# Optimization experiments

Hardware: AMD Instinct MI355X
Metric: run time of the kernel (lower is better)

## Reference

```python
import jax, jax.numpy as jnp
import numpy as np

N, E, D, G, C = 50000, 800000, 128, 64, 2
SCALE = 1.0 / np.sqrt(D).astype(np.float32)


def setup_inputs() -> dict:
    key = jax.random.key(0)
    ks = jax.random.split(key, 32)
    inp = {
        "x": jax.random.normal(ks[0], (N, D), dtype=jnp.float32),
        "edge_index": jax.random.randint(ks[1], (2, E), 0, N),
        "batch": jnp.sort(jax.random.randint(ks[2], (N,), 0, G)),
    }
    i = 3
    for l in range(2):
        for nm in ("Wq", "Wk", "Wv", "Ws"):
            inp[f"{nm}{l}"] = jax.random.normal(ks[i], (D, D), dtype=jnp.float32) * 0.05
            i += 1
        for nm in ("bq", "bk", "bv", "bs"):
            inp[f"{nm}{l}"] = jnp.zeros((D,), dtype=jnp.float32)
    inp["Wc1"] = jax.random.normal(ks[i], (D // 2, D), dtype=jnp.float32) * 0.05
    inp["bc1"] = jnp.zeros((D // 2,), dtype=jnp.float32)
    inp["Wc2"] = jax.random.normal(ks[i + 1], (C, D // 2), dtype=jnp.float32) * 0.05
    inp["bc2"] = jnp.zeros((C,), dtype=jnp.float32)
    return inp


def _transformer_conv(x, src, dst, Wq, bq, Wk, bk, Wv, bv, Ws, bs):
    # PyG TransformerConv, heads=1, concat=True, root_weight=True, beta=False.
    q = x @ Wq.T + bq            # [N, D] node-level projections, then gather per edge
    k = x @ Wk.T + bk
    v = x @ Wv.T + bv
    alpha = jnp.sum(q[dst] * k[src], axis=-1) * SCALE          # [E]
    # segment softmax over incoming edges of each target node
    m = jax.ops.segment_max(alpha, dst, num_segments=N)         # [N]
    ea = jnp.exp(alpha - m[dst])
    denom = jax.ops.segment_sum(ea, dst, num_segments=N)        # [N]
    w = ea / denom[dst]                                         # [E]
    out = jax.ops.segment_sum(v[src] * w[:, None], dst, num_segments=N)  # [N, D]
    return out + x @ Ws.T + bs   # skip connection (lin_skip)


def reference(x, edge_index, batch,
              Wq0, bq0, Wk0, bk0, Wv0, bv0, Ws0, bs0,
              Wq1, bq1, Wk1, bk1, Wv1, bv1, Ws1, bs1,
              Wc1, bc1, Wc2, bc2):
    src, dst = edge_index[0], edge_index[1]
    h = _transformer_conv(x, src, dst, Wq0, bq0, Wk0, bk0, Wv0, bv0, Ws0, bs0)
    h = jax.nn.relu(h)  # dropout is a no-op in eval mode
    h = _transformer_conv(h, src, dst, Wq1, bq1, Wk1, bk1, Wv1, bv1, Ws1, bs1)
    h = jax.nn.relu(h)
    # global mean pool over graphs
    sums = jax.ops.segment_sum(h, batch, num_segments=G)        # [G, D]
    cnts = jax.ops.segment_sum(jnp.ones((h.shape[0],), h.dtype), batch, num_segments=G)
    pooled = sums / jnp.maximum(cnts, 1.0)[:, None]
    # classifier MLP: [D -> D//2 -> C]
    z = jax.nn.relu(pooled @ Wc1.T + bc1)
    return z @ Wc2.T + bc2
```

## Files before the change

kernel.cpp:

```cpp
#include <hip/hip_runtime.h>
#include <math.h>

typedef __bf16 bf16x8 __attribute__((ext_vector_type(8)));
typedef float  f32x4  __attribute__((ext_vector_type(4)));
typedef float  f32x2  __attribute__((ext_vector_type(2)));
typedef unsigned short ushort_t;
typedef unsigned short ushort8 __attribute__((ext_vector_type(8)));

constexpr int Nn = 50000;
constexpr int Ee = 800000;
constexpr int Dd = 128;
constexpr int Gg = 64;
constexpr float SCALE = 0.08838834764831845f;
constexpr float QS    = 16.0f;
constexpr float ISC   = SCALE / (QS * QS);

__device__ inline ushort_t f2bf(float f) {
    unsigned u = __float_as_uint(f);
    unsigned r = (u + 0x7FFF + ((u >> 16) & 1)) >> 16;
    return (ushort_t)r;
}
__device__ inline float bf2f(ushort_t b) { return __uint_as_float(((unsigned)b) << 16); }

__device__ inline char q_i8(float f) {
    int v = (int)rintf(f * QS);
    v = max(-127, min(127, v));
    return (char)v;
}


constexpr int EB  = (Ee + 255) / 256;
constexpr int NBD = (Nn + 255) / 256;
constexpr int CWB = 64;
constexpr int N4  = Nn * Dd / 4;
constexpr int CXB = N4 / 256;

__global__ __launch_bounds__(256) void prep_kernel(
    const int* __restrict__ dst, int* __restrict__ counts, int* __restrict__ rank,
    const int* __restrict__ batch, int* __restrict__ startg, int* __restrict__ endg,
    const float* w0, const float* w1, const float* w2, const float* w3,
    const float* w4, const float* w5, const float* w6, const float* w7,
    ushort_t* __restrict__ Wfh, ushort_t* __restrict__ Wfl,
    const float* __restrict__ x, ushort_t* __restrict__ Xh, ushort_t* __restrict__ Xl) {
    int b = blockIdx.x;
    if (b < EB) {
        int e = b * 256 + threadIdx.x;
        if (e < Ee) rank[e] = atomicAdd(&counts[dst[e]], 1);
    } else if (b < EB + NBD) {
        int n = (b - EB) * 256 + threadIdx.x;
        if (n >= Nn) return;
        int g = batch[n];
        if (n == Nn - 1 || batch[n + 1] != g) endg[g] = n + 1;
        if (n == 0 || batch[n - 1] != g) startg[g] = n;
    } else if (b < EB + NBD + CWB) {
        const float* ws[8] = {w0, w1, w2, w3, w4, w5, w6, w7};
        int b2 = b - (EB + NBD);
        int m = b2 >> 3;
        int tt = (b2 & 7) * 256 + threadIdx.x;
        int lane = tt & 63;
        int ln = lane & 15, quad = lane >> 4;
        int n = (tt >> 9) * 32 + ((tt >> 8) & 1) * 16 + ln;
        int k0 = ((tt >> 6) & 3) * 32 + quad * 8;
        const float* srcp = ws[m] + n * 128 + k0;
        float4 a = *(const float4*)(srcp);
        float4 bb = *(const float4*)(srcp + 4);
        float e[8] = {a.x, a.y, a.z, a.w, bb.x, bb.y, bb.z, bb.w};
        ushort8 h, l;
#pragma unroll
        for (int j = 0; j < 8; ++j) {
            h[j] = f2bf(e[j]);
            l[j] = f2bf(e[j] - bf2f(h[j]));
        }
        size_t o = (size_t)m * 16384 + (size_t)tt * 8;
        *(ushort8*)(Wfh + o) = h;
        *(ushort8*)(Wfl + o) = l;
    } else {
        int i = (b - (EB + NBD + CWB)) * 256 + threadIdx.x;
        if (i >= N4) return;
        float4 xv = ((const float4*)x)[i];
        ushort4 h, l;
        h.x = f2bf(xv.x); l.x = f2bf(xv.x - bf2f(h.x));
        h.y = f2bf(xv.y); l.y = f2bf(xv.y - bf2f(h.y));
        h.z = f2bf(xv.z); l.z = f2bf(xv.z - bf2f(h.z));
        h.w = f2bf(xv.w); l.w = f2bf(xv.w - bf2f(h.w));
        ((ushort4*)Xh)[i] = h;
        ((ushort4*)Xl)[i] = l;
    }
}


__global__ __launch_bounds__(256) void scan1_kernel(const int* __restrict__ counts,
                                                    int* __restrict__ offsets,
                                                    int* __restrict__ blockSums) {
    __shared__ int sh[256];
    int i = blockIdx.x * 256 + threadIdx.x;
    int v = (i < Nn) ? counts[i] : 0;
    sh[threadIdx.x] = v;
    __syncthreads();
    for (int off = 1; off < 256; off <<= 1) {
        int t = (threadIdx.x >= off) ? sh[threadIdx.x - off] : 0;
        __syncthreads();
        sh[threadIdx.x] += t;
        __syncthreads();
    }
    if (i < Nn) offsets[i] = sh[threadIdx.x] - v;
    if (threadIdx.x == 255) blockSums[blockIdx.x] = sh[255];
}

__global__ __launch_bounds__(256) void scan2_kernel(int* __restrict__ blockSums, int nb) {
    __shared__ int sh[256];
    int t = threadIdx.x;
    int v = (t < nb) ? blockSums[t] : 0;
    sh[t] = v;
    __syncthreads();
    for (int off = 1; off < 256; off <<= 1) {
        int u = (t >= off) ? sh[t - off] : 0;
        __syncthreads();
        sh[t] += u;
        __syncthreads();
    }
    if (t < nb) blockSums[t] = sh[t] - v;
}

__global__ __launch_bounds__(256) void scan3_kernel(int* __restrict__ offsets,
                                                    const int* __restrict__ blockSums) {
    int i = blockIdx.x * 256 + threadIdx.x;
    if (i < Nn) offsets[i] += blockSums[blockIdx.x];
    if (i == 0) offsets[Nn] = Ee;
}


constexpr int XS = 136;

__device__ __attribute__((always_inline)) void gemm_body(int bx, int which,
    const ushort_t* __restrict__ Xh, const ushort_t* __restrict__ Xl,
    const ushort_t* __restrict__ Wfh, const ushort_t* __restrict__ Wfl,
    int lw,
    const float* __restrict__ b0, const float* __restrict__ b1,
    const float* __restrict__ b2, const float* __restrict__ b3,
    char* __restrict__ Oq, char* __restrict__ Okv,
    ushort_t* __restrict__ Os) {
    __shared__ ushort_t XhS[64 * XS];
    __shared__ ushort_t XlS[64 * XS];
    const ushort_t* wfh = Wfh + (size_t)(lw + which) * 16384;
    const ushort_t* wfl = Wfl + (size_t)(lw + which) * 16384;
    const float* bias = (which == 0) ? b0 : (which == 1) ? b1 : (which == 2) ? b2 : b3;
    char* O8 = (which == 0) ? Oq : (which == 1) ? Okv : Okv + 128;
    int   o8str = (which == 0) ? 128 : 256;

    int w = threadIdx.x >> 6;
    int lane = threadIdx.x & 63;
    int quad = lane >> 4, ln = lane & 15;
    int n0 = w * 32;

    bf16x8 bh[2][4], bl[2][4];
#pragma unroll
    for (int ct = 0; ct < 2; ++ct)
#pragma unroll
        for (int kc = 0; kc < 4; ++kc) {
            int off = (w * 512 + ct * 256 + kc * 64 + lane) * 8;
            bh[ct][kc] = *(const bf16x8*)(wfh + off);
            bl[ct][kc] = *(const bf16x8*)(wfl + off);
        }
    float bias0 = bias[n0 + ln];
    float bias1 = bias[n0 + 16 + ln];

    int rowBase = bx * 256;
    int trow = threadIdx.x >> 4;
    int tcol = (threadIdx.x & 15) * 8;

    for (int chunk = 0; chunk < 4; ++chunk) {
        int cbase = rowBase + chunk * 64;
        __syncthreads();
#pragma unroll
        for (int rr = 0; rr < 4; ++rr) {
            int lrow = trow + rr * 16;
            int grow = min(cbase + lrow, Nn - 1);
            *(ushort8*)(&XhS[lrow * XS + tcol]) =
                *(const ushort8*)(Xh + (size_t)grow * 128 + tcol);
            *(ushort8*)(&XlS[lrow * XS + tcol]) =
                *(const ushort8*)(Xl + (size_t)grow * 128 + tcol);
        }
        __syncthreads();

#pragma unroll
        for (int rt = 0; rt < 4; ++rt) {
            const ushort_t* ph = &XhS[(rt * 16 + ln) * XS + quad * 8];
            const ushort_t* pl = &XlS[(rt * 16 + ln) * XS + quad * 8];
            bf16x8 ah[4], al[4];
#pragma unroll
            for (int kc = 0; kc < 4; ++kc) {
                ah[kc] = *(const bf16x8*)(ph + kc * 32);
                al[kc] = *(const bf16x8*)(pl + kc * 32);
            }
            f32x4 acc00 = {0.f,0.f,0.f,0.f}, acc01 = {0.f,0.f,0.f,0.f};
            f32x4 acc10 = {0.f,0.f,0.f,0.f}, acc11 = {0.f,0.f,0.f,0.f};
#pragma unroll
            for (int kc = 0; kc < 2; ++kc) {
                int k2 = kc + 2;
                acc00 = __builtin_amdgcn_mfma_f32_16x16x32_bf16(ah[kc], bh[0][kc], acc00, 0, 0, 0);
                acc01 = __builtin_amdgcn_mfma_f32_16x16x32_bf16(ah[kc], bh[1][kc], acc01, 0, 0, 0);
                acc10 = __builtin_amdgcn_mfma_f32_16x16x32_bf16(ah[k2], bh[0][k2], acc10, 0, 0, 0);
                acc11 = __builtin_amdgcn_mfma_f32_16x16x32_bf16(ah[k2], bh[1][k2], acc11, 0, 0, 0);
                acc00 = __builtin_amdgcn_mfma_f32_16x16x32_bf16(ah[kc], bl[0][kc], acc00, 0, 0, 0);
                acc01 = __builtin_amdgcn_mfma_f32_16x16x32_bf16(ah[kc], bl[1][kc], acc01, 0, 0, 0);
                acc10 = __builtin_amdgcn_mfma_f32_16x16x32_bf16(ah[k2], bl[0][k2], acc10, 0, 0, 0);
                acc11 = __builtin_amdgcn_mfma_f32_16x16x32_bf16(ah[k2], bl[1][k2], acc11, 0, 0, 0);
                acc00 = __builtin_amdgcn_mfma_f32_16x16x32_bf16(al[kc], bh[0][kc], acc00, 0, 0, 0);
                acc01 = __builtin_amdgcn_mfma_f32_16x16x32_bf16(al[kc], bh[1][kc], acc01, 0, 0, 0);
                acc10 = __builtin_amdgcn_mfma_f32_16x16x32_bf16(al[k2], bh[0][k2], acc10, 0, 0, 0);
                acc11 = __builtin_amdgcn_mfma_f32_16x16x32_bf16(al[k2], bh[1][k2], acc11, 0, 0, 0);
            }
            int m0 = cbase + rt * 16;
            int orow0 = m0 + quad * 4;
            bool full = (orow0 + 3) < Nn;
#pragma unroll
            for (int reg = 0; reg < 4; ++reg) {
                int orow = orow0 + reg;
                if (full || orow < Nn) {
                    float o0 = acc00[reg] + acc10[reg] + bias0;
                    float o1 = acc01[reg] + acc11[reg] + bias1;
                    if (which <= 1) {
                        size_t ob = (size_t)orow * o8str;
                        O8[ob + n0 + ln]      = q_i8(o0);
                        O8[ob + n0 + 16 + ln] = q_i8(o1);
                    } else if (which == 2) {
                        int pk = __builtin_amdgcn_cvt_pk_fp8_f32(o0, o1, 0, false);
                        size_t ob = (size_t)orow * 256;
                        O8[ob + n0 + ln]      = (char)(pk & 0xff);
                        O8[ob + n0 + 16 + ln] = (char)((pk >> 8) & 0xff);
                    } else {
                        size_t ob = (size_t)orow * 128;
                        Os[ob + n0 + ln]      = f2bf(o0);
                        Os[ob + n0 + 16 + ln] = f2bf(o1);
                    }
                }
            }
        }
    }
}

__global__ __launch_bounds__(256) void gemm_mfma_kernel(
    const ushort_t* __restrict__ Xh, const ushort_t* __restrict__ Xl,
    const ushort_t* __restrict__ Wfh, const ushort_t* __restrict__ Wfl,
    int lw,
    const float* __restrict__ b0, const float* __restrict__ b1,
    const float* __restrict__ b2, const float* __restrict__ b3,
    char* __restrict__ Oq, char* __restrict__ Okv,
    ushort_t* __restrict__ Os) {
    gemm_body(blockIdx.x, blockIdx.y, Xh, Xl, Wfh, Wfl, lw, b0, b1, b2, b3, Oq, Okv, Os);
}

constexpr int G0B = 196 * 4;

__global__ __launch_bounds__(256) void gemm0_scatter_kernel(
    const ushort_t* __restrict__ Xh, const ushort_t* __restrict__ Xl,
    const ushort_t* __restrict__ Wfh, const ushort_t* __restrict__ Wfl,
    const float* __restrict__ b0, const float* __restrict__ b1,
    const float* __restrict__ b2, const float* __restrict__ b3,
    char* __restrict__ Oq, char* __restrict__ Okv, ushort_t* __restrict__ Os,
    const int* __restrict__ src, const int* __restrict__ dst,
    const int* __restrict__ offsets, const int* __restrict__ rank,
    int* __restrict__ sorted_src) {
    int b = blockIdx.x;
    if (b >= G0B) {
        int e = (b - G0B) * 256 + threadIdx.x;
        if (e < Ee) sorted_src[offsets[dst[e]] + rank[e]] = src[e];
        return;
    }
    gemm_body(b % 196, b / 196, Xh, Xl, Wfh, Wfl, 0, b0, b1, b2, b3, Oq, Okv, Os);
}


__global__ __launch_bounds__(256) void attn_kernel(const char* __restrict__ q,
                                                   const char* __restrict__ kv,
                                                   const ushort_t* __restrict__ s,
                                                   const int* __restrict__ offsets,
                                                   const int* __restrict__ sorted_src,
                                                   ushort_t* __restrict__ oh,
                                                   ushort_t* __restrict__ ol,
                                                   int write_split) {
    __shared__ float merge[4][8][128];
    int warp = threadIdx.x >> 6;
    int wid = blockIdx.x * 4 + warp;
    if (wid >= Nn) return;
    int lane = threadIdx.x & 63;
    int g = lane >> 3;
    int gl = lane & 7;
    int4 qw = *(const int4*)(q + (size_t)wid * 128 + gl * 16);
    int beg = offsets[wid], end = offsets[wid + 1];

    float l = 0.f;
    f32x4 accq[4];
#pragma unroll
    for (int j = 0; j < 4; ++j) accq[j] = (f32x4){0.f, 0.f, 0.f, 0.f};
    f32x2* acc = (f32x2*)accq;

    int e = beg + g;
    int s0 = (e < end) ? sorted_src[e] : 0;
    int s1 = (e + 8 < end) ? sorted_src[e + 8] : 0;
    const char* kvp0 = kv + (size_t)s0 * 256 + gl * 16;
    int4 kw = *(const int4*)(kvp0);
    int4 vw = *(const int4*)(kvp0 + 128);

    for (; e < end; e += 8) {
        const char* kvp1 = kv + (size_t)s1 * 256 + gl * 16;
        int4 kw1 = *(const int4*)(kvp1);
        int4 vw1 = *(const int4*)(kvp1 + 128);
        int s2 = (e + 16 < end) ? sorted_src[e + 16] : 0;

        int di = __builtin_amdgcn_sdot4(qw.x, kw.x, 0, false);
        di = __builtin_amdgcn_sdot4(qw.y, kw.y, di, false);
        di = __builtin_amdgcn_sdot4(qw.z, kw.z, di, false);
        di = __builtin_amdgcn_sdot4(qw.w, kw.w, di, false);
        di += __shfl_xor(di, 1, 64);
        di += __shfl_xor(di, 2, 64);
        di += __shfl_xor(di, 4, 64);
        float pw = __expf((float)di * ISC);
        l += pw;
        f32x2 pw2 = {pw, pw};
        {
            f32x2 lo, hi;
            lo = __builtin_amdgcn_cvt_pk_f32_fp8(vw.x, false);
            hi = __builtin_amdgcn_cvt_pk_f32_fp8(vw.x, true);
            acc[0] += pw2 * lo; acc[1] += pw2 * hi;
            lo = __builtin_amdgcn_cvt_pk_f32_fp8(vw.y, false);
            hi = __builtin_amdgcn_cvt_pk_f32_fp8(vw.y, true);
            acc[2] += pw2 * lo; acc[3] += pw2 * hi;
            lo = __builtin_amdgcn_cvt_pk_f32_fp8(vw.z, false);
            hi = __builtin_amdgcn_cvt_pk_f32_fp8(vw.z, true);
            acc[4] += pw2 * lo; acc[5] += pw2 * hi;
            lo = __builtin_amdgcn_cvt_pk_f32_fp8(vw.w, false);
            hi = __builtin_amdgcn_cvt_pk_f32_fp8(vw.w, true);
            acc[6] += pw2 * lo; acc[7] += pw2 * hi;
        }
        kw = kw1; vw = vw1; s1 = s2;
    }

    float* mrow = &merge[warp][g][gl * 16];
    *(f32x4*)(mrow + 0)  = accq[0];
    *(f32x4*)(mrow + 4)  = accq[1];
    *(f32x4*)(mrow + 8)  = accq[2];
    *(f32x4*)(mrow + 12) = accq[3];
    __builtin_amdgcn_sched_barrier(0);
    asm volatile("s_waitcnt lgkmcnt(0)" ::: "memory");
    __builtin_amdgcn_sched_barrier(0);

    l += __shfl_xor(l, 8, 64);
    l += __shfl_xor(l, 16, 64);
    l += __shfl_xor(l, 32, 64);

    int d0 = lane << 1;
    f32x2 sum = {0.f, 0.f};
#pragma unroll
    for (int gg = 0; gg < 8; ++gg) sum += *(f32x2*)(&merge[warp][gg][d0]);

    float inv = (l > 0.f) ? (1.0f / l) : 0.f;
    ushort2 sv = *(const ushort2*)(s + (size_t)wid * 128 + d0);
    float o0 = fmaxf(sum.x * inv + bf2f(sv.x), 0.f);
    float o1 = fmaxf(sum.y * inv + bf2f(sv.y), 0.f);
    ushort2 h;
    h.x = f2bf(o0); h.y = f2bf(o1);
    *(ushort2*)(oh + (size_t)wid * 128 + d0) = h;
    if (write_split) {
        ushort2 lo2;
        lo2.x = f2bf(o0 - bf2f(h.x));
        lo2.y = f2bf(o1 - bf2f(h.y));
        *(ushort2*)(ol + (size_t)wid * 128 + d0) = lo2;
    }
}


__global__ __launch_bounds__(256) void pool_kernel(const ushort_t* __restrict__ hb,
                                                   const int* __restrict__ batch,
                                                   float* __restrict__ pooled) {
    __shared__ float ps[4][128];
    int n0 = blockIdx.x * 256;
    int t = threadIdx.x;
    int lane32 = t & 31, rowgrp = t >> 5;
    for (int i = t; i < 512; i += 256) ((float*)ps)[i] = 0.f;
    __syncthreads();
    int gfirst = batch[min(n0, Nn - 1)];
    int d0 = lane32 * 4;
    float a0 = 0.f, a1 = 0.f, a2 = 0.f, a3 = 0.f;
    int curg = -1;
    for (int rr = 0; rr < 32; ++rr) {
        int n = n0 + rowgrp + rr * 8;
        if (n >= Nn) break;
        int g = batch[n];
        if (g != curg) {
            if (curg >= 0) {
                int slot = curg - gfirst;
                if (slot < 4) {
                    atomicAdd(&ps[slot][d0],     a0);
                    atomicAdd(&ps[slot][d0 + 1], a1);
                    atomicAdd(&ps[slot][d0 + 2], a2);
                    atomicAdd(&ps[slot][d0 + 3], a3);
                } else {
                    atomicAdd(&pooled[curg * Dd + d0],     a0);
                    atomicAdd(&pooled[curg * Dd + d0 + 1], a1);
                    atomicAdd(&pooled[curg * Dd + d0 + 2], a2);
                    atomicAdd(&pooled[curg * Dd + d0 + 3], a3);
                }
                a0 = a1 = a2 = a3 = 0.f;
            }
            curg = g;
        }
        ushort4 hv = *(const ushort4*)(hb + (size_t)n * 128 + d0);
        a0 += bf2f(hv.x); a1 += bf2f(hv.y); a2 += bf2f(hv.z); a3 += bf2f(hv.w);
    }
    if (curg >= 0) {
        int slot = curg - gfirst;
        if (slot < 4) {
            atomicAdd(&ps[slot][d0],     a0);
            atomicAdd(&ps[slot][d0 + 1], a1);
            atomicAdd(&ps[slot][d0 + 2], a2);
            atomicAdd(&ps[slot][d0 + 3], a3);
        } else {
            atomicAdd(&pooled[curg * Dd + d0],     a0);
            atomicAdd(&pooled[curg * Dd + d0 + 1], a1);
            atomicAdd(&pooled[curg * Dd + d0 + 2], a2);
            atomicAdd(&pooled[curg * Dd + d0 + 3], a3);
        }
    }
    __syncthreads();
    int glast = batch[min(n0 + 255, Nn - 1)];
    int nslots = min(glast - gfirst + 1, 4);
    for (int i = t; i < nslots * 128; i += 256) {
        int slot = i >> 7, d = i & 127;
        atomicAdd(&pooled[(gfirst + slot) * Dd + d], ps[slot][d]);
    }
}

__global__ __launch_bounds__(64) void mlp_kernel(const float* __restrict__ pooled,
                                                 const int* __restrict__ startg,
                                                 const int* __restrict__ endg,
                                                 const float* __restrict__ Wc1,
                                                 const float* __restrict__ bc1,
                                                 const float* __restrict__ Wc2,
                                                 const float* __restrict__ bc2,
                                                 float* __restrict__ out) {
    __shared__ float pm[128];
    __shared__ float hid[64];
    int g = blockIdx.x, t = threadIdx.x;
    float cnt = fmaxf((float)(endg[g] - startg[g]), 1.0f);
    float invc = 1.0f / cnt;
    pm[t]      = pooled[g * 128 + t] * invc;
    pm[t + 64] = pooled[g * 128 + 64 + t] * invc;
    __syncthreads();
    float acc = bc1[t];
    for (int i = 0; i < 128; ++i) acc += pm[i] * Wc1[t * 128 + i];
    hid[t] = fmaxf(acc, 0.f);
    __syncthreads();
    if (t < 2) {
        float a = bc2[t];
        for (int i = 0; i < 64; ++i) a += hid[i] * Wc2[t * 64 + i];
        out[g * 2 + t] = a;
    }
}


extern "C" void kernel_launch(void* const* d_in, const int* in_sizes, int n_in,
                              void* d_out, int out_size, void* d_ws, size_t ws_size,
                              hipStream_t stream) {
    const float* x   = (const float*)d_in[0];
    const int*   ei  = (const int*)d_in[1];
    const int* batch = (const int*)d_in[2];
    const float* W[2][4];
    const float* B[2][4];
    for (int l = 0; l < 2; ++l) {
        for (int j = 0; j < 4; ++j) W[l][j] = (const float*)d_in[3 + l * 8 + j];
        for (int j = 0; j < 4; ++j) B[l][j] = (const float*)d_in[3 + l * 8 + 4 + j];
    }
    const float* Wc1 = (const float*)d_in[19];
    const float* bc1 = (const float*)d_in[20];
    const float* Wc2 = (const float*)d_in[21];
    const float* bc2 = (const float*)d_in[22];
    float* out = (float*)d_out;

    const int* src = ei;
    const int* dst = ei + Ee;

    char* p = (char*)d_ws;
    auto alloc = [&](size_t bytes) {
        void* r = (void*)p;
        p += (bytes + 255) & ~(size_t)255;
        return r;
    };
    char*     q  = (char*)alloc((size_t)Nn * 128);
    char*     kv = (char*)alloc((size_t)Nn * 256);
    ushort_t* ss = (ushort_t*)alloc((size_t)Nn * 128 * 2);
    ushort_t* hb = (ushort_t*)alloc((size_t)Nn * 128 * 2);
    ushort_t* Xh = (ushort_t*)alloc((size_t)Nn * 128 * 2);
    ushort_t* Xl = (ushort_t*)alloc((size_t)Nn * 128 * 2);
    ushort_t* Wfh = (ushort_t*)alloc((size_t)8 * 16384 * 2);
    ushort_t* Wfl = (ushort_t*)alloc((size_t)8 * 16384 * 2);
    char* zbase = p;
    int*   counts = (int*)alloc(Nn * 4);
    int*   startg = (int*)alloc(Gg * 4);
    int*   endg   = (int*)alloc(Gg * 4);
    float* pooled = (float*)alloc(Gg * Dd * 4);
    size_t zbytes = (size_t)(p - zbase);
    int* offsets    = (int*)alloc((size_t)(Nn + 1) * 4);
    int* rank       = (int*)alloc((size_t)Ee * 4);
    int* blockSums  = (int*)alloc(256 * 4);
    int* sorted_src = (int*)alloc((size_t)Ee * 4);

    hipMemsetAsync(zbase, 0, zbytes, stream);

    constexpr int NB = (Nn + 255) / 256;

    prep_kernel<<<EB + NBD + CWB + CXB, 256, 0, stream>>>(
        dst, counts, rank, batch, startg, endg,
        W[0][0], W[0][1], W[0][2], W[0][3], W[1][0], W[1][1], W[1][2], W[1][3],
        Wfh, Wfl, x, Xh, Xl);
    scan1_kernel<<<NB, 256, 0, stream>>>(counts, offsets, blockSums);
    scan2_kernel<<<1, 256, 0, stream>>>(blockSums, NB);
    scan3_kernel<<<NB, 256, 0, stream>>>(offsets, blockSums);

    gemm0_scatter_kernel<<<G0B + EB, 256, 0, stream>>>(
        Xh, Xl, Wfh, Wfl, B[0][0], B[0][1], B[0][2], B[0][3],
        q, kv, ss, src, dst, offsets, rank, sorted_src);

    attn_kernel<<<(Nn + 3) / 4, 256, 0, stream>>>(q, kv, ss, offsets, sorted_src,
                                                  Xh, Xl, 1);
    dim3 ggrid(196, 4);
    gemm_mfma_kernel<<<ggrid, 256, 0, stream>>>(Xh, Xl, Wfh, Wfl, 4,
                                                B[1][0], B[1][1], B[1][2], B[1][3],
                                                q, kv, ss);
    attn_kernel<<<(Nn + 3) / 4, 256, 0, stream>>>(q, kv, ss, offsets, sorted_src,
                                                  hb, hb, 0);

    pool_kernel<<<(Nn + 255) / 256, 256, 0, stream>>>(hb, batch, pooled);
    mlp_kernel<<<Gg, 64, 0, stream>>>(pooled, startg, endg, Wc1, bc1, Wc2, bc2, out);
}
```

Measured before the change: 314.3 us.

## Load GEMM A-operands directly from global memory and widen X split conversion

The projection GEMM no longer stages 64-row chunks of Xh/Xl through shared memory with block barriers. Each wave now loads its bf16x8 A fragments straight from global memory per 16-row tile, unrolled by four. This removes LDS traffic and __syncthreads, but all four waves now reload the same rows, which leans on L1/L2 hits. The X hi/lo bf16 split in prep now handles 8 elements per thread with 16-byte stores instead of 4.

```diff
diff --git a/kernel.cpp b/kernel.cpp
--- a/kernel.cpp
+++ b/kernel.cpp
@@ -32,8 +32,8 @@
 constexpr int EB  = (Ee + 255) / 256;
 constexpr int NBD = (Nn + 255) / 256;
 constexpr int CWB = 64;
-constexpr int N4  = Nn * Dd / 4;
-constexpr int CXB = N4 / 256;
+constexpr int N8  = Nn * Dd / 8;
+constexpr int CXB = N8 / 256;
 
 __global__ __launch_bounds__(256) void prep_kernel(
     const int* __restrict__ dst, int* __restrict__ counts, int* __restrict__ rank,
@@ -76,15 +76,18 @@
         *(ushort8*)(Wfl + o) = l;
     } else {
         int i = (b - (EB + NBD + CWB)) * 256 + threadIdx.x;
-        if (i >= N4) return;
-        float4 xv = ((const float4*)x)[i];
-        ushort4 h, l;
-        h.x = f2bf(xv.x); l.x = f2bf(xv.x - bf2f(h.x));
-        h.y = f2bf(xv.y); l.y = f2bf(xv.y - bf2f(h.y));
-        h.z = f2bf(xv.z); l.z = f2bf(xv.z - bf2f(h.z));
-        h.w = f2bf(xv.w); l.w = f2bf(xv.w - bf2f(h.w));
-        ((ushort4*)Xh)[i] = h;
-        ((ushort4*)Xl)[i] = l;
+        if (i >= N8) return;
+        float4 xa = ((const float4*)x)[i * 2];
+        float4 xb = ((const float4*)x)[i * 2 + 1];
+        float e[8] = {xa.x, xa.y, xa.z, xa.w, xb.x, xb.y, xb.z, xb.w};
+        ushort8 h, l;
+#pragma unroll
+        for (int j = 0; j < 8; ++j) {
+            h[j] = f2bf(e[j]);
+            l[j] = f2bf(e[j] - bf2f(h[j]));
+        }
+        ((ushort8*)Xh)[i] = h;
+        ((ushort8*)Xl)[i] = l;
     }
 }
 
@@ -130,8 +133,6 @@
 }
 
 
-constexpr int XS = 136;
-
 __device__ __attribute__((always_inline)) void gemm_body(int bx, int which,
     const ushort_t* __restrict__ Xh, const ushort_t* __restrict__ Xl,
     const ushort_t* __restrict__ Wfh, const ushort_t* __restrict__ Wfl,
@@ -140,8 +141,6 @@
     const float* __restrict__ b2, const float* __restrict__ b3,
     char* __restrict__ Oq, char* __restrict__ Okv,
     ushort_t* __restrict__ Os) {
-    __shared__ ushort_t XhS[64 * XS];
-    __shared__ ushort_t XlS[64 * XS];
     const ushort_t* wfh = Wfh + (size_t)(lw + which) * 16384;
     const ushort_t* wfl = Wfl + (size_t)(lw + which) * 16384;
     const float* bias = (which == 0) ? b0 : (which == 1) ? b1 : (which == 2) ? b2 : b3;
@@ -166,74 +165,58 @@
     float bias1 = bias[n0 + 16 + ln];
 
     int rowBase = bx * 256;
-    int trow = threadIdx.x >> 4;
-    int tcol = (threadIdx.x & 15) * 8;
-
-    for (int chunk = 0; chunk < 4; ++chunk) {
-        int cbase = rowBase + chunk * 64;
-        __syncthreads();
-#pragma unroll
-        for (int rr = 0; rr < 4; ++rr) {
-            int lrow = trow + rr * 16;
-            int grow = min(cbase + lrow, Nn - 1);
-            *(ushort8*)(&XhS[lrow * XS + tcol]) =
-                *(const ushort8*)(Xh + (size_t)grow * 128 + tcol);
-            *(ushort8*)(&XlS[lrow * XS + tcol]) =
-                *(const ushort8*)(Xl + (size_t)grow * 128 + tcol);
-        }
-        __syncthreads();
-
-#pragma unroll
-        for (int rt = 0; rt < 4; ++rt) {
-            const ushort_t* ph = &XhS[(rt * 16 + ln) * XS + quad * 8];
-            const ushort_t* pl = &XlS[(rt * 16 + ln) * XS + quad * 8];
-            bf16x8 ah[4], al[4];
-#pragma unroll
-            for (int kc = 0; kc < 4; ++kc) {
-                ah[kc] = *(const bf16x8*)(ph + kc * 32);
-                al[kc] = *(const bf16x8*)(pl + kc * 32);
-            }
-            f32x4 acc00 = {0.f,0.f,0.f,0.f}, acc01 = {0.f,0.f,0.f,0.f};
-            f32x4 acc10 = {0.f,0.f,0.f,0.f}, acc11 = {0.f,0.f,0.f,0.f};
-#pragma unroll
-            for (int kc = 0; kc < 2; ++kc) {
-                int k2 = kc + 2;
-                acc00 = __builtin_amdgcn_mfma_f32_16x16x32_bf16(ah[kc], bh[0][kc], acc00, 0, 0, 0);
-                acc01 = __builtin_amdgcn_mfma_f32_16x16x32_bf16(ah[kc], bh[1][kc], acc01, 0, 0, 0);
-                acc10 = __builtin_amdgcn_mfma_f32_16x16x32_bf16(ah[k2], bh[0][k2], acc10, 0, 0, 0);
-                acc11 = __builtin_amdgcn_mfma_f32_16x16x32_bf16(ah[k2], bh[1][k2], acc11, 0, 0, 0);
-                acc00 = __builtin_amdgcn_mfma_f32_16x16x32_bf16(ah[kc], bl[0][kc], acc00, 0, 0, 0);
-                acc01 = __builtin_amdgcn_mfma_f32_16x16x32_bf16(ah[kc], bl[1][kc], acc01, 0, 0, 0);
-                acc10 = __builtin_amdgcn_mfma_f32_16x16x32_bf16(ah[k2], bl[0][k2], acc10, 0, 0, 0);
-                acc11 = __builtin_amdgcn_mfma_f32_16x16x32_bf16(ah[k2], bl[1][k2], acc11, 0, 0, 0);
-                acc00 = __builtin_amdgcn_mfma_f32_16x16x32_bf16(al[kc], bh[0][kc], acc00, 0, 0, 0);
-                acc01 = __builtin_amdgcn_mfma_f32_16x16x32_bf16(al[kc], bh[1][kc], acc01, 0, 0, 0);
-                acc10 = __builtin_amdgcn_mfma_f32_16x16x32_bf16(al[k2], bh[0][k2], acc10, 0, 0, 0);
-                acc11 = __builtin_amdgcn_mfma_f32_16x16x32_bf16(al[k2], bh[1][k2], acc11, 0, 0, 0);
-            }
-            int m0 = cbase + rt * 16;
-            int orow0 = m0 + quad * 4;
-            bool full = (orow0 + 3) < Nn;
-#pragma unroll
-            for (int reg = 0; reg < 4; ++reg) {
-                int orow = orow0 + reg;
-                if (full || orow < Nn) {
-                    float o0 = acc00[reg] + acc10[reg] + bias0;
-                    float o1 = acc01[reg] + acc11[reg] + bias1;
-                    if (which <= 1) {
-                        size_t ob = (size_t)orow * o8str;
-                        O8[ob + n0 + ln]      = q_i8(o0);
-                        O8[ob + n0 + 16 + ln] = q_i8(o1);
-                    } else if (which == 2) {
-                        int pk = __builtin_amdgcn_cvt_pk_fp8_f32(o0, o1, 0, false);
-                        size_t ob = (size_t)orow * 256;
-                        O8[ob + n0 + ln]      = (char)(pk & 0xff);
-                        O8[ob + n0 + 16 + ln] = (char)((pk >> 8) & 0xff);
-                    } else {
-                        size_t ob = (size_t)orow * 128;
-                        Os[ob + n0 + ln]      = f2bf(o0);
-                        Os[ob + n0 + 16 + ln] = f2bf(o1);
-                    }
+
+#pragma unroll 4
+    for (int rt = 0; rt < 16; ++rt) {
+        int m0 = rowBase + rt * 16;
+        int grow = min(m0 + ln, Nn - 1);
+        const ushort_t* ph = Xh + (size_t)grow * 128 + quad * 8;
+        const ushort_t* pl = Xl + (size_t)grow * 128 + quad * 8;
+        bf16x8 ah[4], al[4];
+#pragma unroll
+        for (int kc = 0; kc < 4; ++kc) {
+            ah[kc] = *(const bf16x8*)(ph + kc * 32);
+            al[kc] = *(const bf16x8*)(pl + kc * 32);
+        }
+        f32x4 acc00 = {0.f,0.f,0.f,0.f}, acc01 = {0.f,0.f,0.f,0.f};
+        f32x4 acc10 = {0.f,0.f,0.f,0.f}, acc11 = {0.f,0.f,0.f,0.f};
+#pragma unroll
+        for (int kc = 0; kc < 2; ++kc) {
+            int k2 = kc + 2;
+            acc00 = __builtin_amdgcn_mfma_f32_16x16x32_bf16(ah[kc], bh[0][kc], acc00, 0, 0, 0);
+            acc01 = __builtin_amdgcn_mfma_f32_16x16x32_bf16(ah[kc], bh[1][kc], acc01, 0, 0, 0);
+            acc10 = __builtin_amdgcn_mfma_f32_16x16x32_bf16(ah[k2], bh[0][k2], acc10, 0, 0, 0);
+            acc11 = __builtin_amdgcn_mfma_f32_16x16x32_bf16(ah[k2], bh[1][k2], acc11, 0, 0, 0);
+            acc00 = __builtin_amdgcn_mfma_f32_16x16x32_bf16(ah[kc], bl[0][kc], acc00, 0, 0, 0);
+            acc01 = __builtin_amdgcn_mfma_f32_16x16x32_bf16(ah[kc], bl[1][kc], acc01, 0, 0, 0);
+            acc10 = __builtin_amdgcn_mfma_f32_16x16x32_bf16(ah[k2], bl[0][k2], acc10, 0, 0, 0);
+            acc11 = __builtin_amdgcn_mfma_f32_16x16x32_bf16(ah[k2], bl[1][k2], acc11, 0, 0, 0);
+            acc00 = __builtin_amdgcn_mfma_f32_16x16x32_bf16(al[kc], bh[0][kc], acc00, 0, 0, 0);
+            acc01 = __builtin_amdgcn_mfma_f32_16x16x32_bf16(al[kc], bh[1][kc], acc01, 0, 0, 0);
+            acc10 = __builtin_amdgcn_mfma_f32_16x16x32_bf16(al[k2], bh[0][k2], acc10, 0, 0, 0);
+            acc11 = __builtin_amdgcn_mfma_f32_16x16x32_bf16(al[k2], bh[1][k2], acc11, 0, 0, 0);
+        }
+        int orow0 = m0 + quad * 4;
+        bool full = (orow0 + 3) < Nn;
+#pragma unroll
+        for (int reg = 0; reg < 4; ++reg) {
+            int orow = orow0 + reg;
+            if (full || orow < Nn) {
+                float o0 = acc00[reg] + acc10[reg] + bias0;
+                float o1 = acc01[reg] + acc11[reg] + bias1;
+                if (which <= 1) {
+                    size_t ob = (size_t)orow * o8str;
+                    O8[ob + n0 + ln]      = q_i8(o0);
+                    O8[ob + n0 + 16 + ln] = q_i8(o1);
+                } else if (which == 2) {
+                    int pk = __builtin_amdgcn_cvt_pk_fp8_f32(o0, o1, 0, false);
+                    size_t ob = (size_t)orow * 256;
+                    O8[ob + n0 + ln]      = (char)(pk & 0xff);
+                    O8[ob + n0 + 16 + ln] = (char)((pk >> 8) & 0xff);
+                } else {
+                    size_t ob = (size_t)orow * 128;
+                    Os[ob + n0 + ln]      = f2bf(o0);
+                    Os[ob + n0 + 16 + ln] = f2bf(o1);
                 }
             }
         }
```

After: 373.3 us. 1.19x slower.
